# Performance work log

Hardware: AMD Instinct MI355X
Metric: run time of the kernel (lower is better)

Reference implementation:

```python
import jax, jax.numpy as jnp
import numpy as np

# ---- constants matching init_kwargs ----
N_ELEMENT = 8
N_LINES = 32
LINES_PER_ELEM = 4  # n_line_group_each_element = [4]*8
MINIBATCH = 512
SAMPLE_N = 1024
SAMPLE_CM = 0.01
PROBE_I0 = 100000.0
SIGNAL_ATT = 1.0
DET_SOLID_ANGLE_RATIO = 0.05
N_VOXEL_MB = MINIBATCH * SAMPLE_N


def setup_inputs() -> dict:
    key = jax.random.key(0)
    k1, k2, k3, k4 = jax.random.split(key, 4)
    xp = jax.random.uniform(k1, (N_ELEMENT, MINIBATCH, SAMPLE_N), dtype=jnp.float32)
    mu_probe = jax.random.uniform(k2, (N_ELEMENT,), dtype=jnp.float32)
    fl_unit = jax.random.uniform(k3, (N_LINES,), dtype=jnp.float32)
    SA_theta = jax.random.uniform(k4, (N_LINES, N_VOXEL_MB), dtype=jnp.float32)
    return {"xp": xp, "mu_probe": mu_probe, "fl_unit": fl_unit, "SA_theta": SA_theta}


def reference(xp, mu_probe, fl_unit, SA_theta):
    # xp: (E, B, N) concentration minibatch, theta==0 so rotation is skipped.
    conc = xp  # (E, B, N)

    # Probe attenuation: per-element LAC, prefix-sum along beam axis,
    # zero-padded at entry face, summed over elements.
    lac = conc * mu_probe[:, None, None]                     # (E, B, N)
    lac_acc = jnp.cumsum(lac, axis=-1)                       # (E, B, N)
    zeros_col = jnp.zeros((N_ELEMENT, MINIBATCH, 1), dtype=conc.dtype)
    lac_acc = jnp.concatenate([zeros_col, lac_acc], axis=-1) # (E, B, N+1)
    att_exponent_acc_map = jnp.sum(lac_acc, axis=0) * (SAMPLE_CM / SAMPLE_N)  # (B, N+1)

    # Fluorescence map: line l belongs to element l // LINES_PER_ELEM.
    elem_of_line = jnp.repeat(jnp.arange(N_ELEMENT), LINES_PER_ELEM)  # (L,) const
    conc_flat = conc.reshape(N_ELEMENT, N_VOXEL_MB)                   # (E, V)
    fl_map_tot = conc_flat[elem_of_line] * fl_unit[:, None]           # (L, V)

    attenuation_flat = jnp.exp(-att_exponent_acc_map[:, :-1]).reshape(N_VOXEL_MB)
    transmission_att_exponent = att_exponent_acc_map[:, -1]           # (B,)

    probe_after_att = PROBE_I0 * attenuation_flat                     # (V,)
    fl_signal = probe_after_att[None, :] * fl_map_tot * SA_theta      # (L, V)
    fl_signal = fl_signal.reshape(N_LINES, MINIBATCH, SAMPLE_N).sum(axis=-1)
    fl_signal = fl_signal * DET_SOLID_ANGLE_RATIO * SIGNAL_ATT        # (L, B)

    return fl_signal, transmission_att_exponent
```

## Files before the change

kernel.cpp:

```cpp
#include <hip/hip_runtime.h>

constexpr int NE = 8;
constexpr int NL = 32;
constexpr int MB = 512;
constexpr int SN = 1024;
constexpr float KS   = 0.01f / 1024.0f;
constexpr float I0   = 100000.0f;
constexpr float OUTS = 0.05f;

__global__ __launch_bounds__(256)
void ppm_kernel(const float* __restrict__ xp,
                const float* __restrict__ mu,
                const float* __restrict__ fl,
                const float* __restrict__ SA,
                float* __restrict__ out)
{
    const int b    = blockIdx.x;
    const int t    = threadIdx.x;
    const int lane = t & 63;
    const int wv   = t >> 6;

    __shared__ float s_wave[4];
    __shared__ float s_acc[256 * 33];
    __shared__ float s_part[256];

    float x[NE][4];
    #pragma unroll
    for (int e = 0; e < NE; ++e) {
        const float4 v = reinterpret_cast<const float4*>(
            xp + (size_t)e * (MB * SN) + (size_t)b * SN)[t];
        x[e][0] = v.x; x[e][1] = v.y; x[e][2] = v.z; x[e][3] = v.w;
    }

    float a0 = 0.f, a1 = 0.f, a2 = 0.f, a3 = 0.f;
    #pragma unroll
    for (int e = 0; e < NE; ++e) {
        const float m = mu[e];
        a0 = fmaf(m, x[e][0], a0);
        a1 = fmaf(m, x[e][1], a1);
        a2 = fmaf(m, x[e][2], a2);
        a3 = fmaf(m, x[e][3], a3);
    }

    const float e1 = a0, e2 = a0 + a1, e3 = e2 + a2;
    const float T  = e3 + a3;

    float incl = T;
    #pragma unroll
    for (int d = 1; d < 64; d <<= 1) {
        const float v = __shfl_up(incl, d, 64);
        if (lane >= d) incl += v;
    }
    if (lane == 63) s_wave[wv] = incl;
    __syncthreads();

    float woff = 0.f;
    for (int w2 = 0; w2 < wv; ++w2) woff += s_wave[w2];
    const float bex = woff + (incl - T);

    if (t == 0) {
        out[NL * MB + b] = KS * (s_wave[0] + s_wave[1] + s_wave[2] + s_wave[3]);
    }

    const float w0 = I0 * __expf(-KS * bex);
    const float w1 = I0 * __expf(-KS * (bex + e1));
    const float w2 = I0 * __expf(-KS * (bex + e2));
    const float w3 = I0 * __expf(-KS * (bex + e3));
    #pragma unroll
    for (int e = 0; e < NE; ++e) {
        x[e][0] *= w0; x[e][1] *= w1; x[e][2] *= w2; x[e][3] *= w3;
    }

    const size_t sabase = (size_t)b * SN;
    #pragma unroll 8
    for (int l = 0; l < NL; ++l) {
        const float4 sa = reinterpret_cast<const float4*>(
            SA + (size_t)l * (size_t)(MB * SN) + sabase)[t];
        const int e = l >> 2;
        const float acc = x[e][0] * sa.x + x[e][1] * sa.y
                        + x[e][2] * sa.z + x[e][3] * sa.w;
        s_acc[t * 33 + l] = acc;
    }
    __syncthreads();

    {
        const int l = t & 31, g = t >> 5;
        float s = 0.f;
        #pragma unroll
        for (int j = 0; j < 32; ++j) s += s_acc[(g * 32 + j) * 33 + l];
        s_part[t] = s;
    }
    __syncthreads();

    if (t < 32) {
        float tot = 0.f;
        #pragma unroll
        for (int g2 = 0; g2 < 8; ++g2) tot += s_part[g2 * 32 + t];
        out[t * MB + b] = OUTS * fl[t] * tot;
    }
}

extern "C" void kernel_launch(void* const* d_in, const int* in_sizes, int n_in,
                              void* d_out, int out_size, void* d_ws, size_t ws_size,
                              hipStream_t stream) {
    const float* xp = (const float*)d_in[0];
    const float* mu = (const float*)d_in[1];
    const float* fl = (const float*)d_in[2];
    const float* SA = (const float*)d_in[3];
    float* out = (float*)d_out;
    ppm_kernel<<<MB, 256, 0, stream>>>(xp, mu, fl, SA, out);
}
```

Baseline: 18.44 us.

## Use 1024-thread blocks with per-wave line reductions via shared weighted concentrations

Blocks grow from 256 to 1024 threads, with one voxel per thread for the prefix scan. Each thread stores its attenuation-weighted concentrations in shared memory. Each of the 16 waves then handles two fluorescence lines, reading SA as float4 and reducing with wave shuffles. This drops the large padded shared transpose buffer and the two-stage block reduction, and raises parallelism. The cost is an extra shared-memory round trip for the weighted concentrations and more waves per block, which lowers occupancy flexibility.

Measured after the change: 19.83 us. 7.5% more time.

```diff
diff --git a/kernel.cpp b/kernel.cpp
--- a/kernel.cpp
+++ b/kernel.cpp
@@ -8,7 +8,7 @@
 constexpr float I0   = 100000.0f;
 constexpr float OUTS = 0.05f;
 
-__global__ __launch_bounds__(256)
+__global__ __launch_bounds__(1024)
 void ppm_kernel(const float* __restrict__ xp,
                 const float* __restrict__ mu,
                 const float* __restrict__ fl,
@@ -20,32 +20,18 @@
     const int lane = t & 63;
     const int wv   = t >> 6;
 
-    __shared__ float s_wave[4];
-    __shared__ float s_acc[256 * 33];
-    __shared__ float s_part[256];
+    __shared__ float s_wave[16];
+    __shared__ float s_wx[NE][SN];
 
-    float x[NE][4];
+    float x[NE];
+    float a = 0.f;
     #pragma unroll
     for (int e = 0; e < NE; ++e) {
-        const float4 v = reinterpret_cast<const float4*>(
-            xp + (size_t)e * (MB * SN) + (size_t)b * SN)[t];
-        x[e][0] = v.x; x[e][1] = v.y; x[e][2] = v.z; x[e][3] = v.w;
+        x[e] = xp[(size_t)e * (MB * SN) + (size_t)b * SN + t];
+        a = fmaf(mu[e], x[e], a);
     }
 
-    float a0 = 0.f, a1 = 0.f, a2 = 0.f, a3 = 0.f;
-    #pragma unroll
-    for (int e = 0; e < NE; ++e) {
-        const float m = mu[e];
-        a0 = fmaf(m, x[e][0], a0);
-        a1 = fmaf(m, x[e][1], a1);
-        a2 = fmaf(m, x[e][2], a2);
-        a3 = fmaf(m, x[e][3], a3);
-    }
-
-    const float e1 = a0, e2 = a0 + a1, e3 = e2 + a2;
-    const float T  = e3 + a3;
-
-    float incl = T;
+    float incl = a;
     #pragma unroll
     for (int d = 1; d < 64; d <<= 1) {
         const float v = __shfl_up(incl, d, 64);
@@ -55,48 +41,40 @@
     __syncthreads();
 
     float woff = 0.f;
-    for (int w2 = 0; w2 < wv; ++w2) woff += s_wave[w2];
-    const float bex = woff + (incl - T);
+    #pragma unroll
+    for (int w2 = 0; w2 < 16; ++w2) woff += (w2 < wv) ? s_wave[w2] : 0.f;
+    const float pex = woff + (incl - a);
+    const float w   = I0 * __expf(-KS * pex);
 
     if (t == 0) {
-        out[NL * MB + b] = KS * (s_wave[0] + s_wave[1] + s_wave[2] + s_wave[3]);
+        float tot = 0.f;
+        #pragma unroll
+        for (int w2 = 0; w2 < 16; ++w2) tot += s_wave[w2];
+        out[NL * MB + b] = KS * tot;
     }
 
-    const float w0 = I0 * __expf(-KS * bex);
-    const float w1 = I0 * __expf(-KS * (bex + e1));
-    const float w2 = I0 * __expf(-KS * (bex + e2));
-    const float w3 = I0 * __expf(-KS * (bex + e3));
     #pragma unroll
-    for (int e = 0; e < NE; ++e) {
-        x[e][0] *= w0; x[e][1] *= w1; x[e][2] *= w2; x[e][3] *= w3;
-    }
-
-    const size_t sabase = (size_t)b * SN;
-    #pragma unroll 8
-    for (int l = 0; l < NL; ++l) {
-        const float4 sa = reinterpret_cast<const float4*>(
-            SA + (size_t)l * (size_t)(MB * SN) + sabase)[t];
-        const int e = l >> 2;
-        const float acc = x[e][0] * sa.x + x[e][1] * sa.y
-                        + x[e][2] * sa.z + x[e][3] * sa.w;
-        s_acc[t * 33 + l] = acc;
-    }
+    for (int e = 0; e < NE; ++e) s_wx[e][t] = w * x[e];
     __syncthreads();
 
-    {
-        const int l = t & 31, g = t >> 5;
-        float s = 0.f;
+    #pragma unroll
+    for (int li = 0; li < 2; ++li) {
+        const int l = wv + 16 * li;
+        const int e = l >> 2;
+        const float4* sa4 = reinterpret_cast<const float4*>(
+            SA + (size_t)l * (size_t)(MB * SN) + (size_t)b * SN);
+        const float4* wx4 = reinterpret_cast<const float4*>(&s_wx[e][0]);
+        float acc = 0.f;
         #pragma unroll
-        for (int j = 0; j < 32; ++j) s += s_acc[(g * 32 + j) * 33 + l];
-        s_part[t] = s;
-    }
-    __syncthreads();
-
-    if (t < 32) {
-        float tot = 0.f;
+        for (int j = 0; j < 4; ++j) {
+            const int idx = lane + 64 * j;
+            const float4 sa = sa4[idx];
+            const float4 wx = wx4[idx];
+            acc += wx.x * sa.x + wx.y * sa.y + wx.z * sa.z + wx.w * sa.w;
+        }
         #pragma unroll
-        for (int g2 = 0; g2 < 8; ++g2) tot += s_part[g2 * 32 + t];
-        out[t * MB + b] = OUTS * fl[t] * tot;
+        for (int d = 32; d >= 1; d >>= 1) acc += __shfl_down(acc, d, 64);
+        if (lane == 0) out[l * MB + b] = OUTS * fl[l] * acc;
     }
 }
 
@@ -108,5 +86,5 @@
     const float* fl = (const float*)d_in[2];
     const float* SA = (const float*)d_in[3];
     float* out = (float*)d_out;
-    ppm_kernel<<<MB, 256, 0, stream>>>(xp, mu, fl, SA, out);
+    ppm_kernel<<<MB, 1024, 0, stream>>>(xp, mu, fl, SA, out);
 }
```

## Split into scan kernel writing bf16 weighted conc and wave-per-row dot kernel

Applied to the files above, without the earlier changes.

Splits the fused kernel in two. The first kernel does the prefix-sum attenuation and writes the attenuation-weighted concentration to workspace as bf16. The second kernel assigns one wavefront per (line, batch) row and computes the SA dot product with a shuffle reduction. This drops the large shared-memory transpose and raises parallelism for the dominant SA read. In exchange it adds a second launch, an extra write and read of an 8 MB bf16 intermediate, and bf16 rounding error.

Measured after the change: 22.61 us. +22.6%, slower.

```diff
diff --git a/kernel.cpp b/kernel.cpp
--- a/kernel.cpp
+++ b/kernel.cpp
@@ -8,12 +8,20 @@
 constexpr float I0   = 100000.0f;
 constexpr float OUTS = 0.05f;
 
+__device__ __forceinline__ unsigned short f2bf(float f) {
+    unsigned u = __float_as_uint(f);
+    u += 0x7FFFu + ((u >> 16) & 1u);
+    return (unsigned short)(u >> 16);
+}
+__device__ __forceinline__ float bf2f(unsigned short h) {
+    return __uint_as_float(((unsigned)h) << 16);
+}
+
 __global__ __launch_bounds__(256)
-void ppm_kernel(const float* __restrict__ xp,
-                const float* __restrict__ mu,
-                const float* __restrict__ fl,
-                const float* __restrict__ SA,
-                float* __restrict__ out)
+void ppm_scan_kernel(const float* __restrict__ xp,
+                     const float* __restrict__ mu,
+                     unsigned short* __restrict__ wx,
+                     float* __restrict__ out)
 {
     const int b    = blockIdx.x;
     const int t    = threadIdx.x;
@@ -21,8 +29,6 @@
     const int wv   = t >> 6;
 
     __shared__ float s_wave[4];
-    __shared__ float s_acc[256 * 33];
-    __shared__ float s_part[256];
 
     float x[NE][4];
     #pragma unroll
@@ -41,7 +47,6 @@
         a2 = fmaf(m, x[e][2], a2);
         a3 = fmaf(m, x[e][3], a3);
     }
-
     const float e1 = a0, e2 = a0 + a1, e3 = e2 + a2;
     const float T  = e3 + a3;
 
@@ -55,7 +60,8 @@
     __syncthreads();
 
     float woff = 0.f;
-    for (int w2 = 0; w2 < wv; ++w2) woff += s_wave[w2];
+    #pragma unroll
+    for (int w2 = 0; w2 < 4; ++w2) woff += (w2 < wv) ? s_wave[w2] : 0.f;
     const float bex = woff + (incl - T);
 
     if (t == 0) {
@@ -66,38 +72,48 @@
     const float w1 = I0 * __expf(-KS * (bex + e1));
     const float w2 = I0 * __expf(-KS * (bex + e2));
     const float w3 = I0 * __expf(-KS * (bex + e3));
+
     #pragma unroll
     for (int e = 0; e < NE; ++e) {
-        x[e][0] *= w0; x[e][1] *= w1; x[e][2] *= w2; x[e][3] *= w3;
+        ushort4 o;
+        o.x = f2bf(w0 * x[e][0]);
+        o.y = f2bf(w1 * x[e][1]);
+        o.z = f2bf(w2 * x[e][2]);
+        o.w = f2bf(w3 * x[e][3]);
+        reinterpret_cast<ushort4*>(wx + (size_t)e * (MB * SN) + (size_t)b * SN)[t] = o;
     }
+}
 
-    const size_t sabase = (size_t)b * SN;
-    #pragma unroll 8
-    for (int l = 0; l < NL; ++l) {
-        const float4 sa = reinterpret_cast<const float4*>(
-            SA + (size_t)l * (size_t)(MB * SN) + sabase)[t];
-        const int e = l >> 2;
-        const float acc = x[e][0] * sa.x + x[e][1] * sa.y
-                        + x[e][2] * sa.z + x[e][3] * sa.w;
-        s_acc[t * 33 + l] = acc;
+__global__ __launch_bounds__(256)
+void ppm_dot_kernel(const unsigned short* __restrict__ wx,
+                    const float* __restrict__ fl,
+                    const float* __restrict__ SA,
+                    float* __restrict__ out)
+{
+    const int lane = threadIdx.x & 63;
+    const int wv   = threadIdx.x >> 6;
+    const int p    = blockIdx.x * 4 + wv;
+    const int l    = p >> 9;
+    const int b    = p & 511;
+    const int e    = l >> 2;
+
+    const float4*  sa4 = reinterpret_cast<const float4*>(
+        SA + (size_t)l * (size_t)(MB * SN) + (size_t)b * SN);
+    const ushort4* wx4 = reinterpret_cast<const ushort4*>(
+        wx + (size_t)e * (size_t)(MB * SN) + (size_t)b * SN);
+
+    float acc = 0.f;
+    #pragma unroll
+    for (int j = 0; j < 4; ++j) {
+        const int idx = lane + 64 * j;
+        const float4  sa = sa4[idx];
+        const ushort4 wq = wx4[idx];
+        acc += bf2f(wq.x) * sa.x + bf2f(wq.y) * sa.y
+             + bf2f(wq.z) * sa.z + bf2f(wq.w) * sa.w;
     }
-    __syncthreads();
-
-    {
-        const int l = t & 31, g = t >> 5;
-        float s = 0.f;
-        #pragma unroll
-        for (int j = 0; j < 32; ++j) s += s_acc[(g * 32 + j) * 33 + l];
-        s_part[t] = s;
-    }
-    __syncthreads();
-
-    if (t < 32) {
-        float tot = 0.f;
-        #pragma unroll
-        for (int g2 = 0; g2 < 8; ++g2) tot += s_part[g2 * 32 + t];
-        out[t * MB + b] = OUTS * fl[t] * tot;
-    }
+    #pragma unroll
+    for (int d = 32; d >= 1; d >>= 1) acc += __shfl_down(acc, d, 64);
+    if (lane == 0) out[l * MB + b] = OUTS * fl[l] * acc;
 }
 
 extern "C" void kernel_launch(void* const* d_in, const int* in_sizes, int n_in,
@@ -108,5 +124,8 @@
     const float* fl = (const float*)d_in[2];
     const float* SA = (const float*)d_in[3];
     float* out = (float*)d_out;
-    ppm_kernel<<<MB, 256, 0, stream>>>(xp, mu, fl, SA, out);
+    unsigned short* wx = (unsigned short*)d_ws;
+
+    ppm_scan_kernel<<<MB, 256, 0, stream>>>(xp, mu, wx, out);
+    ppm_dot_kernel<<<NL * MB / 4, 256, 0, stream>>>(wx, fl, SA, out);
 }
```

## Warp-specialize block: scan waves overlap SA prefetch waves, shuffle-reduce per line

Applied to the files above, without the earlier changes.

Grows the block to 768 threads. Four waves load xp and do the prefix scan while eight extra waves, one per element, prefetch their SA rows into registers at the same time. The weighted concentrations go through shared memory, and each element wave does its four line dot products and reduces them with wave shuffles. This replaces the 33-padded shared accumulator and the two-stage block reduction, and it is meant to hide the SA memory latency behind the scan. The cost is much higher register use per block and more threads per block, which may limit occupancy.

After: 22.38 us. +21.3%, slower.

```diff
diff --git a/kernel.cpp b/kernel.cpp
--- a/kernel.cpp
+++ b/kernel.cpp
@@ -8,95 +8,144 @@
 constexpr float I0   = 100000.0f;
 constexpr float OUTS = 0.05f;
 
-__global__ __launch_bounds__(256)
-void ppm_kernel(const float* __restrict__ xp,
-                const float* __restrict__ mu,
-                const float* __restrict__ fl,
-                const float* __restrict__ SA,
-                float* __restrict__ out)
+__global__ __launch_bounds__(768, 6)
+void ppm_fused(const float* __restrict__ xp,
+               const float* __restrict__ mu,
+               const float* __restrict__ fl,
+               const float* __restrict__ SA,
+               float* __restrict__ out)
 {
     const int b    = blockIdx.x;
     const int t    = threadIdx.x;
     const int lane = t & 63;
-    const int wv   = t >> 6;
 
     __shared__ float s_wave[4];
-    __shared__ float s_acc[256 * 33];
-    __shared__ float s_part[256];
+    __shared__ float s_wx[NE][SN];
+
+    const int dw = (t >> 6) - 4;
+    const size_t sarow = (size_t)b * SN;
 
     float x[NE][4];
-    #pragma unroll
-    for (int e = 0; e < NE; ++e) {
-        const float4 v = reinterpret_cast<const float4*>(
-            xp + (size_t)e * (MB * SN) + (size_t)b * SN)[t];
-        x[e][0] = v.x; x[e][1] = v.y; x[e][2] = v.z; x[e][3] = v.w;
+    float4 sa0[4], sa1[4];
+    float e1 = 0.f, e2 = 0.f, e3 = 0.f, T = 0.f, incl = 0.f;
+
+    if (t < 256) {
+        const int wv = t >> 6;
+        #pragma unroll
+        for (int e = 0; e < NE; ++e) {
+            const float4 v = reinterpret_cast<const float4*>(
+                xp + (size_t)e * (MB * SN) + sarow)[t];
+            x[e][0] = v.x; x[e][1] = v.y; x[e][2] = v.z; x[e][3] = v.w;
+        }
+        float a0 = 0.f, a1 = 0.f, a2 = 0.f, a3 = 0.f;
+        #pragma unroll
+        for (int e = 0; e < NE; ++e) {
+            const float m = mu[e];
+            a0 = fmaf(m, x[e][0], a0);
+            a1 = fmaf(m, x[e][1], a1);
+            a2 = fmaf(m, x[e][2], a2);
+            a3 = fmaf(m, x[e][3], a3);
+        }
+        e1 = a0; e2 = a0 + a1; e3 = e2 + a2; T = e3 + a3;
+        incl = T;
+        #pragma unroll
+        for (int d = 1; d < 64; d <<= 1) {
+            const float v = __shfl_up(incl, d, 64);
+            if (lane >= d) incl += v;
+        }
+        if (lane == 63) s_wave[wv] = incl;
+    } else {
+        const float4* sa4a = reinterpret_cast<const float4*>(
+            SA + ((size_t)(4 * dw)     << 19) + sarow);
+        const float4* sa4b = reinterpret_cast<const float4*>(
+            SA + ((size_t)(4 * dw + 1) << 19) + sarow);
+        #pragma unroll
+        for (int j = 0; j < 4; ++j) sa0[j] = sa4a[lane + 64 * j];
+        #pragma unroll
+        for (int j = 0; j < 4; ++j) sa1[j] = sa4b[lane + 64 * j];
     }
 
-    float a0 = 0.f, a1 = 0.f, a2 = 0.f, a3 = 0.f;
-    #pragma unroll
-    for (int e = 0; e < NE; ++e) {
-        const float m = mu[e];
-        a0 = fmaf(m, x[e][0], a0);
-        a1 = fmaf(m, x[e][1], a1);
-        a2 = fmaf(m, x[e][2], a2);
-        a3 = fmaf(m, x[e][3], a3);
+    __syncthreads();
+
+    if (t < 256) {
+        const int wv = t >> 6;
+        float woff = 0.f;
+        #pragma unroll
+        for (int w2 = 0; w2 < 4; ++w2) woff += (w2 < wv) ? s_wave[w2] : 0.f;
+        const float bex = woff + (incl - T);
+
+        if (t == 0) {
+            out[NL * MB + b] = KS * (s_wave[0] + s_wave[1] + s_wave[2] + s_wave[3]);
+        }
+
+        const float w0 = I0 * __expf(-KS * bex);
+        const float w1 = I0 * __expf(-KS * (bex + e1));
+        const float w2 = I0 * __expf(-KS * (bex + e2));
+        const float w3 = I0 * __expf(-KS * (bex + e3));
+
+        #pragma unroll
+        for (int e = 0; e < NE; ++e) {
+            reinterpret_cast<float4*>(&s_wx[e][0])[t] =
+                make_float4(w0 * x[e][0], w1 * x[e][1], w2 * x[e][2], w3 * x[e][3]);
+        }
     }
 
-    const float e1 = a0, e2 = a0 + a1, e3 = e2 + a2;
-    const float T  = e3 + a3;
-
-    float incl = T;
-    #pragma unroll
-    for (int d = 1; d < 64; d <<= 1) {
-        const float v = __shfl_up(incl, d, 64);
-        if (lane >= d) incl += v;
-    }
-    if (lane == 63) s_wave[wv] = incl;
     __syncthreads();
 
-    float woff = 0.f;
-    for (int w2 = 0; w2 < wv; ++w2) woff += s_wave[w2];
-    const float bex = woff + (incl - T);
+    if (t >= 256) {
+        float4 wx[4];
+        const float4* wx4 = reinterpret_cast<const float4*>(&s_wx[dw][0]);
+        #pragma unroll
+        for (int j = 0; j < 4; ++j) wx[j] = wx4[lane + 64 * j];
 
-    if (t == 0) {
-        out[NL * MB + b] = KS * (s_wave[0] + s_wave[1] + s_wave[2] + s_wave[3]);
-    }
+        float acc[4];
 
-    const float w0 = I0 * __expf(-KS * bex);
-    const float w1 = I0 * __expf(-KS * (bex + e1));
-    const float w2 = I0 * __expf(-KS * (bex + e2));
-    const float w3 = I0 * __expf(-KS * (bex + e3));
-    #pragma unroll
-    for (int e = 0; e < NE; ++e) {
-        x[e][0] *= w0; x[e][1] *= w1; x[e][2] *= w2; x[e][3] *= w3;
-    }
+        const float4* sa4c = reinterpret_cast<const float4*>(
+            SA + ((size_t)(4 * dw + 2) << 19) + sarow);
+        float4 sa2[4];
+        #pragma unroll
+        for (int j = 0; j < 4; ++j) sa2[j] = sa4c[lane + 64 * j];
 
-    const size_t sabase = (size_t)b * SN;
-    #pragma unroll 8
-    for (int l = 0; l < NL; ++l) {
-        const float4 sa = reinterpret_cast<const float4*>(
-            SA + (size_t)l * (size_t)(MB * SN) + sabase)[t];
-        const int e = l >> 2;
-        const float acc = x[e][0] * sa.x + x[e][1] * sa.y
-                        + x[e][2] * sa.z + x[e][3] * sa.w;
-        s_acc[t * 33 + l] = acc;
-    }
-    __syncthreads();
+        acc[0] = 0.f; acc[1] = 0.f;
+        #pragma unroll
+        for (int j = 0; j < 4; ++j) {
+            acc[0] += wx[j].x * sa0[j].x + wx[j].y * sa0[j].y
+                    + wx[j].z * sa0[j].z + wx[j].w * sa0[j].w;
+            acc[1] += wx[j].x * sa1[j].x + wx[j].y * sa1[j].y
+                    + wx[j].z * sa1[j].z + wx[j].w * sa1[j].w;
+        }
 
-    {
-        const int l = t & 31, g = t >> 5;
-        float s = 0.f;
+        const float4* sa4d = reinterpret_cast<const float4*>(
+            SA + ((size_t)(4 * dw + 3) << 19) + sarow);
+        float4 sa3[4];
         #pragma unroll
-        for (int j = 0; j < 32; ++j) s += s_acc[(g * 32 + j) * 33 + l];
-        s_part[t] = s;
-    }
-    __syncthreads();
+        for (int j = 0; j < 4; ++j) sa3[j] = sa4d[lane + 64 * j];
 
-    if (t < 32) {
-        float tot = 0.f;
+        acc[2] = 0.f;
         #pragma unroll
-        for (int g2 = 0; g2 < 8; ++g2) tot += s_part[g2 * 32 + t];
-        out[t * MB + b] = OUTS * fl[t] * tot;
+        for (int j = 0; j < 4; ++j) {
+            acc[2] += wx[j].x * sa2[j].x + wx[j].y * sa2[j].y
+                    + wx[j].z * sa2[j].z + wx[j].w * sa2[j].w;
+        }
+        acc[3] = 0.f;
+        #pragma unroll
+        for (int j = 0; j < 4; ++j) {
+            acc[3] += wx[j].x * sa3[j].x + wx[j].y * sa3[j].y
+                    + wx[j].z * sa3[j].z + wx[j].w * sa3[j].w;
+        }
+
+        #pragma unroll
+        for (int li = 0; li < 4; ++li) {
+            #pragma unroll
+            for (int d = 32; d >= 1; d >>= 1) acc[li] += __shfl_down(acc[li], d, 64);
+        }
+        if (lane == 0) {
+            #pragma unroll
+            for (int li = 0; li < 4; ++li) {
+                const int l = 4 * dw + li;
+                out[l * MB + b] = OUTS * fl[l] * acc[li];
+            }
+        }
     }
 }
 
@@ -108,5 +157,5 @@
     const float* fl = (const float*)d_in[2];
     const float* SA = (const float*)d_in[3];
     float* out = (float*)d_out;
-    ppm_kernel<<<MB, 256, 0, stream>>>(xp, mu, fl, SA, out);
+    ppm_fused<<<MB, 768, 0, stream>>>(xp, mu, fl, SA, out);
 }
```
